# Kernel optimization log

Measured on AMD Instinct MI355X. Metric: run time of the kernel, lower is better.

Reference implementation:

```python
import jax, jax.numpy as jnp
import numpy as np

P = 16; N_SIDE = 14; N_PATCH = 196
ENC_DIM = 1024; ENC_DEPTH = 2; ENC_HEADS = 16; ENC_DH = 64
DEC_DIM = 512; DEC_DEPTH = 1; DEC_HEADS = 8; DEC_DH = 64
NUM_MASKED = int(0.75 * N_PATCH)  # 147


def _ln(x, s, b):
    m = jnp.mean(x, axis=-1, keepdims=True)
    v = jnp.var(x, axis=-1, keepdims=True)
    return (x - m) * jax.lax.rsqrt(v + 1e-5) * s + b


def _mha(x, Wqkv, Wo, heads, dh):
    B, N, _ = x.shape
    q, k, v = jnp.split(x @ Wqkv, 3, axis=-1)
    rs = lambda t: t.reshape(B, N, heads, dh).transpose(0, 2, 1, 3)
    q, k, v = rs(q), rs(k), rs(v)
    scores = jnp.einsum('bhqd,bhkd->bhqk', q, k) / jnp.sqrt(jnp.float32(dh))
    att = jax.nn.softmax(scores, axis=-1)
    o = jnp.einsum('bhqk,bhkd->bhqd', att, v).transpose(0, 2, 1, 3).reshape(B, N, heads * dh)
    return o @ Wo


def _transformer(x, params, depth, heads, dh, lnfs, lnfb):
    (ln1s, ln1b, Wqkv, Wo, ln2s, ln2b, W1, b1, W2, b2) = params
    for i in range(depth):
        x = x + _mha(_ln(x, ln1s[i], ln1b[i]), Wqkv[i], Wo[i], heads, dh)
        h = jax.nn.gelu(_ln(x, ln2s[i], ln2b[i]) @ W1[i] + b1[i])
        x = x + h @ W2[i] + b2[i]
    return _ln(x, lnfs, lnfb)


def setup_inputs() -> dict:
    key = jax.random.key(0)
    ks = jax.random.split(key, 24)
    B = 64
    w = lambda k, s: (jax.random.normal(k, s, jnp.float32) * 0.02)
    E, IE = ENC_DIM, ENC_HEADS * ENC_DH
    D, ID = DEC_DIM, DEC_HEADS * DEC_DH
    d = {}
    d['images'] = jax.random.normal(ks[0], (B, 224, 224, 3), jnp.float32)
    d['rand'] = jax.random.uniform(ks[1], (B, N_PATCH), dtype=jnp.float32)
    d['patch_W'] = w(ks[2], (P * P * 3, E)); d['patch_b'] = jnp.zeros((E,), jnp.float32)
    d['pos_emb'] = w(ks[3], (N_PATCH, E))
    d['enc_ln1s'] = jnp.ones((ENC_DEPTH, E), jnp.float32); d['enc_ln1b'] = jnp.zeros((ENC_DEPTH, E), jnp.float32)
    d['enc_Wqkv'] = w(ks[4], (ENC_DEPTH, E, 3 * IE)); d['enc_Wo'] = w(ks[5], (ENC_DEPTH, IE, E))
    d['enc_ln2s'] = jnp.ones((ENC_DEPTH, E), jnp.float32); d['enc_ln2b'] = jnp.zeros((ENC_DEPTH, E), jnp.float32)
    d['enc_W1'] = w(ks[6], (ENC_DEPTH, E, 4 * E)); d['enc_b1'] = jnp.zeros((ENC_DEPTH, 4 * E), jnp.float32)
    d['enc_W2'] = w(ks[7], (ENC_DEPTH, 4 * E, E)); d['enc_b2'] = jnp.zeros((ENC_DEPTH, E), jnp.float32)
    d['enc_lnfs'] = jnp.ones((E,), jnp.float32); d['enc_lnfb'] = jnp.zeros((E,), jnp.float32)
    d['e2d_W'] = w(ks[8], (E, D)); d['e2d_b'] = jnp.zeros((D,), jnp.float32)
    d['mask_token'] = w(ks[9], (D,))
    d['dec_pos'] = w(ks[10], (N_PATCH, D))
    d['dec_ln1s'] = jnp.ones((DEC_DEPTH, D), jnp.float32); d['dec_ln1b'] = jnp.zeros((DEC_DEPTH, D), jnp.float32)
    d['dec_Wqkv'] = w(ks[11], (DEC_DEPTH, D, 3 * ID)); d['dec_Wo'] = w(ks[12], (DEC_DEPTH, ID, D))
    d['dec_ln2s'] = jnp.ones((DEC_DEPTH, D), jnp.float32); d['dec_ln2b'] = jnp.zeros((DEC_DEPTH, D), jnp.float32)
    d['dec_W1'] = w(ks[13], (DEC_DEPTH, D, 4 * D)); d['dec_b1'] = jnp.zeros((DEC_DEPTH, 4 * D), jnp.float32)
    d['dec_W2'] = w(ks[14], (DEC_DEPTH, 4 * D, D)); d['dec_b2'] = jnp.zeros((DEC_DEPTH, D), jnp.float32)
    d['dec_lnfs'] = jnp.ones((D,), jnp.float32); d['dec_lnfb'] = jnp.zeros((D,), jnp.float32)
    d['pix_W'] = w(ks[15], (D, E)); d['pix_b'] = jnp.zeros((E,), jnp.float32)  # pixel_dim == encoder_dim per source
    return d


def reference(images, rand, patch_W, patch_b, pos_emb,
              enc_ln1s, enc_ln1b, enc_Wqkv, enc_Wo, enc_ln2s, enc_ln2b,
              enc_W1, enc_b1, enc_W2, enc_b2, enc_lnfs, enc_lnfb,
              e2d_W, e2d_b, mask_token, dec_pos,
              dec_ln1s, dec_ln1b, dec_Wqkv, dec_Wo, dec_ln2s, dec_ln2b,
              dec_W1, dec_b1, dec_W2, dec_b2, dec_lnfs, dec_lnfb,
              pix_W, pix_b):
    B = images.shape[0]
    # patch embed: [B,224,224,3] -> [B,196,768] -> [B,196,1024]
    x = images.reshape(B, N_SIDE, P, N_SIDE, P, 3).transpose(0, 1, 3, 2, 4, 5).reshape(B, N_PATCH, P * P * 3)
    patches = x @ patch_W + patch_b
    tokens = patches + pos_emb
    # random masking via argsort of uniform noise
    order = jnp.argsort(rand, axis=-1)
    m_idx = order[:, :NUM_MASKED]        # [B,147]
    u_idx = order[:, NUM_MASKED:]        # [B,49]
    unmasked = jnp.take_along_axis(tokens, u_idx[:, :, None], axis=1)
    enc_params = (enc_ln1s, enc_ln1b, enc_Wqkv, enc_Wo, enc_ln2s, enc_ln2b, enc_W1, enc_b1, enc_W2, enc_b2)
    encoded = _transformer(unmasked, enc_params, ENC_DEPTH, ENC_HEADS, ENC_DH, enc_lnfs, enc_lnfb)
    dec_tok = encoded @ e2d_W + e2d_b + dec_pos[u_idx]
    mask_toks = mask_token + dec_pos[m_idx]
    bidx = jnp.arange(B)[:, None]
    all_tok = jnp.zeros((B, N_PATCH, DEC_DIM), dec_tok.dtype)
    all_tok = all_tok.at[bidx, u_idx].set(dec_tok)
    all_tok = all_tok.at[bidx, m_idx].set(mask_toks)
    dec_params = (dec_ln1s, dec_ln1b, dec_Wqkv, dec_Wo, dec_ln2s, dec_ln2b, dec_W1, dec_b1, dec_W2, dec_b2)
    decoded = _transformer(all_tok, dec_params, DEC_DEPTH, DEC_HEADS, DEC_DH, dec_lnfs, dec_lnfb)
    pred = jnp.take_along_axis(decoded, m_idx[:, :, None], axis=1) @ pix_W + pix_b
    target = jnp.take_along_axis(patches, m_idx[:, :, None], axis=1)
    return jnp.mean((pred - target) ** 2)
```

## Files before the change

kernel.cpp:

```cpp
#include <hip/hip_runtime.h>

typedef __attribute__((ext_vector_type(8))) __bf16 bf16x8;
typedef __attribute__((ext_vector_type(4))) float f32x4;

#define OFF_PATCH 0ull
#define OFF_X     25690112ull
#define OFF_LN    51380224ull
#define OFF_QKV   64225280ull
#define OFF_HID   103022592ull
#define OFF_WP    154402816ull
#define OFF_ORD   214695936ull
#define OFF_PART  214746112ull

#define WP_PATCH   0ull
#define WP_ENC_QKV 786432ull
#define WP_ENC_WO  7077888ull
#define WP_ENC_W1  9175040ull
#define WP_ENC_W2  17563648ull
#define WP_E2D     25952256ull
#define WP_DEC_QKV 26476544ull
#define WP_DEC_WO  27262976ull
#define WP_DEC_W1  27525120ull
#define WP_DEC_W2  28573696ull
#define WP_PIX     29622272ull

#define OM_BF16 0
#define OM_F32  1
#define OM_ACC  2
#define OM_GELU 3

__device__ __forceinline__ float b2f(unsigned short u) {
    return __uint_as_float(((unsigned int)u) << 16);
}
__device__ __forceinline__ unsigned short f2b(float f) {
    unsigned int x = __float_as_uint(f);
    x += 0x7fffu + ((x >> 16) & 1u);
    return (unsigned short)(x >> 16);
}
__device__ __forceinline__ float gelu_f(float x) {
    float u2 = 1.5957691216057308f * x * (1.f + 0.044715f * x * x);
    return x / (1.f + __expf(-u2));
}
__device__ __forceinline__ void gload16(const void* g, void* l) {
    __builtin_amdgcn_global_load_lds((const __attribute__((address_space(1))) void*)g,
                                     (__attribute__((address_space(3))) void*)l, 16, 0, 0);
}

__global__ __launch_bounds__(256) void pack_w(const float* __restrict__ in,
                                              unsigned short* __restrict__ out, int K, int N) {
    __shared__ float tile[32][33];
    int kt = blockIdx.y * 32, nt = blockIdx.x * 32;
    int tx = threadIdx.x & 31, ty = threadIdx.x >> 5;
#pragma unroll
    for (int i = 0; i < 32; i += 8) tile[ty + i][tx] = in[(size_t)(kt + ty + i) * N + nt + tx];
    __syncthreads();
#pragma unroll
    for (int i = 0; i < 32; i += 8)
        out[(size_t)(nt + ty + i) * K + kt + tx] = f2b(tile[tx][ty + i]);
}

__global__ __launch_bounds__(256) void patchify_kernel(const float* __restrict__ img,
                                                       unsigned short* __restrict__ Xp) {
    const long long total = 12544ll * 768;
    for (long long e = (long long)blockIdx.x * 256 + threadIdx.x; e < total;
         e += (long long)gridDim.x * 256) {
        int row = (int)(e / 768), k = (int)(e % 768);
        int b = row / 196, pi = row % 196;
        int py = pi / 14, px = pi % 14;
        int r = k / 48, rem = k % 48;
        int c = rem / 3, ch = rem % 3;
        long long src = (((long long)(b * 224 + py * 16 + r)) * 224 + (px * 16 + c)) * 3 + ch;
        Xp[e] = f2b(img[src]);
    }
}

template <int BT, int NW, int OM>
__global__ __launch_bounds__(NW * 64) void gemm2(const unsigned short* __restrict__ A,
                                                 const unsigned short* __restrict__ Bt,
                                                 void* __restrict__ Cv,
                                                 const float* __restrict__ bias,
                                                 int M, int N, int K) {
    constexpr int WN = (BT == 256) ? 4 : 2;
    constexpr int MR = BT / 32;
    __shared__ __align__(16) unsigned short As[2][BT * 64];
    __shared__ __align__(16) unsigned short Bs[2][BT * 64];
    const int tid = threadIdx.x, wave = tid >> 6, lane = tid & 63;
    const int brow = blockIdx.y * BT, bcol = blockIdx.x * BT;
    const int fr = lane & 15, fq = lane >> 4;
    const int wr = (wave / WN) * (MR * 16);
    const int wc = (wave % WN) * 64;
    const int srow = wave * 32 + (lane >> 3);
    const int sca = ((lane & 7) ^ (lane >> 3)) * 8;
    const unsigned short* Ag = A + (size_t)(brow + srow) * K + sca;
    const unsigned short* Bg = Bt + (size_t)(bcol + srow) * K + sca;

    f32x4 acc[MR][4];
#pragma unroll
    for (int m = 0; m < MR; ++m)
#pragma unroll
        for (int n = 0; n < 4; ++n) acc[m][n] = (f32x4){0.f, 0.f, 0.f, 0.f};

    auto stage = [&](int buf, int k0) {
        unsigned short* AsW = &As[buf][(wave * 32) * 64];
        unsigned short* BsW = &Bs[buf][(wave * 32) * 64];
#pragma unroll
        for (int i = 0; i < 4; ++i) {
            gload16(Ag + (size_t)(i * 8) * K + k0, AsW + i * 8 * 64);
            gload16(Bg + (size_t)(i * 8) * K + k0, BsW + i * 8 * 64);
        }
    };
    auto compute = [&](int buf) {
        const char* ab = (const char*)&As[buf][0];
        const char* bb = (const char*)&Bs[buf][0];
        const int sw = (fr & 7) << 4;
#pragma unroll
        for (int kk = 0; kk < 2; ++kk) {
            bf16x8 af[MR], bf[4];
#pragma unroll
            for (int m = 0; m < MR; ++m)
                af[m] = *(const bf16x8*)(ab + (wr + m * 16 + fr) * 128 +
                                         ((kk * 64 + fq * 16) ^ sw));
#pragma unroll
            for (int n = 0; n < 4; ++n)
                bf[n] = *(const bf16x8*)(bb + (wc + n * 16 + fr) * 128 +
                                         ((kk * 64 + fq * 16) ^ sw));
#pragma unroll
            for (int m = 0; m < MR; ++m)
#pragma unroll
                for (int n = 0; n < 4; ++n)
                    acc[m][n] = __builtin_amdgcn_mfma_f32_16x16x32_bf16(af[m], bf[n],
                                                                       acc[m][n], 0, 0, 0);
        }
    };

    const int nt = K >> 6;
    stage(0, 0);
    __syncthreads();
    int cur = 0;
    for (int t = 0; t < nt - 1; ++t) {
        stage(cur ^ 1, (t + 1) << 6);
        compute(cur);
        __syncthreads();
        cur ^= 1;
    }
    compute(cur);

#pragma unroll
    for (int m = 0; m < MR; ++m) {
        int rb = brow + wr + m * 16 + fq * 4;
#pragma unroll
        for (int r = 0; r < 4; ++r) {
            int row = rb + r;
            if (row < M) {
#pragma unroll
                for (int n = 0; n < 4; ++n) {
                    int col = bcol + wc + n * 16 + fr;
                    float v = acc[m][n][r];
                    if (bias) v += bias[col];
                    size_t o = (size_t)row * N + col;
                    if constexpr (OM == OM_BF16) ((unsigned short*)Cv)[o] = f2b(v);
                    else if constexpr (OM == OM_F32) ((float*)Cv)[o] = v;
                    else if constexpr (OM == OM_ACC) ((float*)Cv)[o] += v;
                    else ((unsigned short*)Cv)[o] = f2b(gelu_f(v));
                }
            }
        }
    }
}

template <int N, int H, int NW>
__global__ __launch_bounds__(NW * 64) void attn_mfma(const unsigned short* __restrict__ qkv,
                                                     unsigned short* __restrict__ out) {
    constexpr int Npad = ((N + 31) / 32) * 32;
    constexpr int NT = Npad / 16;
    constexpr int KS = Npad / 32;
    constexpr int PS = Npad + 8;
    constexpr int SQ = 3 * H * 64, SO = H * 64;
    __shared__ __align__(16) unsigned short Kl[Npad * 64];
    __shared__ __align__(16) unsigned short Vt[64 * PS];
    __shared__ __align__(16) unsigned short Pl[NW * 16 * PS];
    const int b = blockIdx.x / H, h = blockIdx.x % H;
    const unsigned short* base = qkv + (size_t)b * N * SQ;
    const int qoff = h * 64, koff = (H + h) * 64, voff = (2 * H + h) * 64;
    const int tid = threadIdx.x, wave = tid >> 6, lane = tid & 63;
    const int fr = lane & 15, fq = lane >> 4;

    for (int idx = tid; idx < Npad * 8; idx += NW * 64) {
        int row = idx >> 3, ch = idx & 7;
        uint4 v = {0u, 0u, 0u, 0u};
        if (row < N) v = *(const uint4*)(base + (size_t)row * SQ + koff + ch * 8);
        *(uint4*)((char*)Kl + row * 128 + ((ch * 16) ^ ((row & 7) << 4))) = v;
    }
    for (int idx = tid; idx < Npad * 32; idx += NW * 64) {
        int key = idx >> 5, d2 = (idx & 31) * 2;
        unsigned int v = 0;
        if (key < N) v = *(const unsigned int*)(base + (size_t)key * SQ + voff + d2);
        Vt[d2 * PS + key] = (unsigned short)(v & 0xffffu);
        Vt[(d2 + 1) * PS + key] = (unsigned short)(v >> 16);
    }
    __syncthreads();

    unsigned short* pw = Pl + wave * 16 * PS;
    for (int qt = wave; qt < NT; qt += NW) {
        const int q0 = qt * 16;
        int qr = q0 + fr;
        if (qr > N - 1) qr = N - 1;
        const unsigned short* qp = base + (size_t)qr * SQ + qoff + fq * 8;
        bf16x8 aq0 = *(const bf16x8*)qp;
        bf16x8 aq1 = *(const bf16x8*)(qp + 32);
        f32x4 sa[NT];
#pragma unroll
        for (int ct = 0; ct < NT; ++ct) sa[ct] = (f32x4){0.f, 0.f, 0.f, 0.f};
#pragma unroll
        for (int ct = 0; ct < NT; ++ct) {
            const char* kb = (const char*)Kl + (ct * 16 + fr) * 128;
            bf16x8 kf0 = *(const bf16x8*)(kb + ((fq * 16) ^ ((fr & 7) << 4)));
            bf16x8 kf1 = *(const bf16x8*)(kb + ((64 + fq * 16) ^ ((fr & 7) << 4)));
            sa[ct] = __builtin_amdgcn_mfma_f32_16x16x32_bf16(aq0, kf0, sa[ct], 0, 0, 0);
            sa[ct] = __builtin_amdgcn_mfma_f32_16x16x32_bf16(aq1, kf1, sa[ct], 0, 0, 0);
        }
        float mrow[4] = {-3e38f, -3e38f, -3e38f, -3e38f};
#pragma unroll
        for (int ct = 0; ct < NT; ++ct) {
            bool ok = (ct * 16 + fr) < N;
#pragma unroll
            for (int r = 0; r < 4; ++r) {
                float s = ok ? sa[ct][r] * 0.125f : -3e38f;
                sa[ct][r] = s;
                mrow[r] = fmaxf(mrow[r], s);
            }
        }
#pragma unroll
        for (int off = 1; off <= 8; off <<= 1)
#pragma unroll
            for (int r = 0; r < 4; ++r) mrow[r] = fmaxf(mrow[r], __shfl_xor(mrow[r], off));
        float ssum[4] = {0.f, 0.f, 0.f, 0.f};
#pragma unroll
        for (int ct = 0; ct < NT; ++ct)
#pragma unroll
            for (int r = 0; r < 4; ++r) {
                float p = __expf(sa[ct][r] - mrow[r]);
                sa[ct][r] = p;
                ssum[r] += p;
            }
#pragma unroll
        for (int off = 1; off <= 8; off <<= 1)
#pragma unroll
            for (int r = 0; r < 4; ++r) ssum[r] += __shfl_xor(ssum[r], off);
#pragma unroll
        for (int ct = 0; ct < NT; ++ct)
#pragma unroll
            for (int r = 0; r < 4; ++r)
                pw[(fq * 4 + r) * PS + ct * 16 + fr] = f2b(sa[ct][r]);
        f32x4 oa[4];
#pragma unroll
        for (int vt = 0; vt < 4; ++vt) oa[vt] = (f32x4){0.f, 0.f, 0.f, 0.f};
#pragma unroll
        for (int ks = 0; ks < KS; ++ks) {
            bf16x8 pa = *(const bf16x8*)(pw + fr * PS + ks * 32 + fq * 8);
#pragma unroll
            for (int vt = 0; vt < 4; ++vt) {
                bf16x8 vf = *(const bf16x8*)(&Vt[(vt * 16 + fr) * PS + ks * 32 + fq * 8]);
                oa[vt] = __builtin_amdgcn_mfma_f32_16x16x32_bf16(pa, vf, oa[vt], 0, 0, 0);
            }
        }
        float inv[4];
#pragma unroll
        for (int r = 0; r < 4; ++r) inv[r] = 1.f / ssum[r];
#pragma unroll
        for (int vt = 0; vt < 4; ++vt)
#pragma unroll
            for (int r = 0; r < 4; ++r) {
                int q = q0 + fq * 4 + r;
                if (q < N)
                    out[((size_t)b * N + q) * SO + h * 64 + vt * 16 + fr] =
                        f2b(oa[vt][r] * inv[r]);
            }
    }
}

__global__ __launch_bounds__(256) void argsort_kernel(const float* __restrict__ rnd,
                                                      int* __restrict__ ord) {
    __shared__ float vals[196];
    int b = blockIdx.x, t = threadIdx.x;
    if (t < 196) vals[t] = rnd[b * 196 + t];
    __syncthreads();
    if (t < 196) {
        float v = vals[t];
        int rank = 0;
        for (int j = 0; j < 196; ++j) {
            float vj = vals[j];
            rank += (vj < v) || (vj == v && j < t);
        }
        ord[b * 196 + rank] = t;
    }
}

__global__ __launch_bounds__(256) void gather_unmasked(const unsigned short* __restrict__ patches,
                                                       const float* __restrict__ pos,
                                                       const int* __restrict__ ord,
                                                       float* __restrict__ xe) {
    int row = blockIdx.x;
    int b = row / 49, i = row % 49;
    int src = ord[b * 196 + 147 + i];
    const unsigned short* pr = patches + ((size_t)(b * 196 + src) << 10);
    const float* pe = pos + ((size_t)src << 10);
    float* o = xe + ((size_t)row << 10);
    int d = threadIdx.x * 4;
    ushort4 pv = *(const ushort4*)(pr + d);
    float4 p4 = *(const float4*)(pe + d);
    float4 r;
    r.x = b2f(pv.x) + p4.x; r.y = b2f(pv.y) + p4.y;
    r.z = b2f(pv.z) + p4.z; r.w = b2f(pv.w) + p4.w;
    *(float4*)(o + d) = r;
}

template <int L>
__global__ __launch_bounds__(256) void ln_kernel(const float* __restrict__ x,
                                                 unsigned short* __restrict__ y,
                                                 const float* __restrict__ sw,
                                                 const float* __restrict__ bw) {
    __shared__ float red[8];
    const int tid = threadIdx.x;
    const float* xr = x + (size_t)blockIdx.x * L;
    float sum = 0.f, sq = 0.f;
    for (int i = tid * 4; i < L; i += 1024) {
        float4 v = *(const float4*)(xr + i);
        sum += v.x + v.y + v.z + v.w;
        sq += v.x * v.x + v.y * v.y + v.z * v.z + v.w * v.w;
    }
    for (int off = 32; off; off >>= 1) {
        sum += __shfl_xor(sum, off);
        sq += __shfl_xor(sq, off);
    }
    int wave = tid >> 6, lane = tid & 63;
    if (lane == 0) { red[wave] = sum; red[4 + wave] = sq; }
    __syncthreads();
    float ts = red[0] + red[1] + red[2] + red[3];
    float tq = red[4] + red[5] + red[6] + red[7];
    float mean = ts / L;
    float inv = rsqrtf(tq / L - mean * mean + 1e-5f);
    unsigned short* yr = y + (size_t)blockIdx.x * L;
    for (int i = tid * 4; i < L; i += 1024) {
        float4 v = *(const float4*)(xr + i);
        float4 s4 = *(const float4*)(sw + i);
        float4 b4 = *(const float4*)(bw + i);
        ushort4 o;
        o.x = f2b((v.x - mean) * inv * s4.x + b4.x);
        o.y = f2b((v.y - mean) * inv * s4.y + b4.y);
        o.z = f2b((v.z - mean) * inv * s4.z + b4.z);
        o.w = f2b((v.w - mean) * inv * s4.w + b4.w);
        *(ushort4*)(yr + i) = o;
    }
}

__global__ __launch_bounds__(256) void scatter_tokens(const float* __restrict__ dec_tok,
                                                      const float* __restrict__ dec_pos,
                                                      const float* __restrict__ mask_tok,
                                                      const int* __restrict__ ord,
                                                      float* __restrict__ all_tok) {
    int e = blockIdx.x;
    int b = e / 196, i = e % 196;
    int idx = ord[e];
    float* o = all_tok + ((size_t)(b * 196 + idx)) * 512;
    const float* dp = dec_pos + (size_t)idx * 512;
    int d = threadIdx.x * 4;
    if (d < 512) {
        float4 dv = *(const float4*)(dp + d);
        float4 sv;
        if (i < 147) sv = *(const float4*)(mask_tok + d);
        else sv = *(const float4*)(dec_tok + ((size_t)(b * 49 + (i - 147))) * 512 + d);
        float4 r = {sv.x + dv.x, sv.y + dv.y, sv.z + dv.z, sv.w + dv.w};
        *(float4*)(o + d) = r;
    }
}

__global__ __launch_bounds__(256) void gather_masked(const unsigned short* __restrict__ x,
                                                     const int* __restrict__ ord,
                                                     unsigned short* __restrict__ gm) {
    int r = blockIdx.x;
    int b = r / 147, j = r % 147;
    int idx = ord[b * 196 + j];
    const unsigned short* src = x + ((size_t)(b * 196 + idx)) * 512;
    unsigned short* o = gm + (size_t)r * 512;
    int d = threadIdx.x * 4;
    if (d < 512) *(ushort4*)(o + d) = *(const ushort4*)(src + d);
}

__global__ __launch_bounds__(256) void loss_partial(const float* __restrict__ pred,
                                                    const unsigned short* __restrict__ patches,
                                                    const int* __restrict__ ord,
                                                    float* __restrict__ part) {
    __shared__ float red[8];
    float local = 0.f;
    const long long total = 9633792ll;
    for (long long e = (long long)blockIdx.x * 256 + threadIdx.x; e < total; e += 4096ll * 256) {
        int r = (int)(e >> 10), d = (int)(e & 1023);
        int b = r / 147, j = r % 147;
        int idx = ord[b * 196 + j];
        float t = b2f(patches[(((size_t)(b * 196 + idx)) << 10) + d]);
        float df = pred[e] - t;
        local += df * df;
    }
    for (int off = 32; off; off >>= 1) local += __shfl_xor(local, off);
    int wave = threadIdx.x >> 6, lane = threadIdx.x & 63;
    if (lane == 0) red[wave] = local;
    __syncthreads();
    if (threadIdx.x == 0) part[blockIdx.x] = red[0] + red[1] + red[2] + red[3];
}

__global__ __launch_bounds__(256) void loss_final(const float* __restrict__ part,
                                                  float* __restrict__ out) {
    __shared__ float red[8];
    float local = 0.f;
    for (int i = threadIdx.x; i < 4096; i += 256) local += part[i];
    for (int off = 32; off; off >>= 1) local += __shfl_xor(local, off);
    int wave = threadIdx.x >> 6, lane = threadIdx.x & 63;
    if (lane == 0) red[wave] = local;
    __syncthreads();
    if (threadIdx.x == 0) out[0] = (red[0] + red[1] + red[2] + red[3]) / 9633792.0f;
}

extern "C" void kernel_launch(void* const* d_in, const int* in_sizes, int n_in, void* d_out,
                              int out_size, void* d_ws, size_t ws_size, hipStream_t stream) {
    const float* images = (const float*)d_in[0];
    const float* rnd = (const float*)d_in[1];
    const float* patch_W = (const float*)d_in[2];
    const float* patch_b = (const float*)d_in[3];
    const float* pos_emb = (const float*)d_in[4];
    const float* enc_ln1s = (const float*)d_in[5];
    const float* enc_ln1b = (const float*)d_in[6];
    const float* enc_Wqkv = (const float*)d_in[7];
    const float* enc_Wo = (const float*)d_in[8];
    const float* enc_ln2s = (const float*)d_in[9];
    const float* enc_ln2b = (const float*)d_in[10];
    const float* enc_W1 = (const float*)d_in[11];
    const float* enc_b1 = (const float*)d_in[12];
    const float* enc_W2 = (const float*)d_in[13];
    const float* enc_b2 = (const float*)d_in[14];
    const float* enc_lnfs = (const float*)d_in[15];
    const float* enc_lnfb = (const float*)d_in[16];
    const float* e2d_W = (const float*)d_in[17];
    const float* e2d_b = (const float*)d_in[18];
    const float* mask_tok = (const float*)d_in[19];
    const float* dec_pos = (const float*)d_in[20];
    const float* dec_ln1s = (const float*)d_in[21];
    const float* dec_ln1b = (const float*)d_in[22];
    const float* dec_Wqkv = (const float*)d_in[23];
    const float* dec_Wo = (const float*)d_in[24];
    const float* dec_ln2s = (const float*)d_in[25];
    const float* dec_ln2b = (const float*)d_in[26];
    const float* dec_W1 = (const float*)d_in[27];
    const float* dec_b1 = (const float*)d_in[28];
    const float* dec_W2 = (const float*)d_in[29];
    const float* dec_b2 = (const float*)d_in[30];
    const float* dec_lnfs = (const float*)d_in[31];
    const float* dec_lnfb = (const float*)d_in[32];
    const float* pix_W = (const float*)d_in[33];
    const float* pix_b = (const float*)d_in[34];

    char* ws = (char*)d_ws;
    unsigned short* patches = (unsigned short*)(ws + OFF_PATCH);
    float* Rx = (float*)(ws + OFF_X);
    unsigned short* Rln = (unsigned short*)(ws + OFF_LN);
    unsigned short* RqkvB = (unsigned short*)(ws + OFF_QKV);
    float* RqkvF = (float*)(ws + OFF_QKV);
    unsigned short* Rhid = (unsigned short*)(ws + OFF_HID);
    unsigned short* wp = (unsigned short*)(ws + OFF_WP);
    int* ord = (int*)(ws + OFF_ORD);
    float* part = (float*)(ws + OFF_PART);
    float* out = (float*)d_out;

    auto PACK = [&](const float* src, size_t wpo, int K, int N) {
        pack_w<<<dim3(N / 32, K / 32), 256, 0, stream>>>(src, wp + wpo, K, N);
    };
    PACK(patch_W, WP_PATCH, 768, 1024);
    for (int l = 0; l < 2; ++l) {
        PACK(enc_Wqkv + (size_t)l * 1024 * 3072, WP_ENC_QKV + (size_t)l * 3145728, 1024, 3072);
        PACK(enc_Wo + (size_t)l * 1024 * 1024, WP_ENC_WO + (size_t)l * 1048576, 1024, 1024);
        PACK(enc_W1 + (size_t)l * 1024 * 4096, WP_ENC_W1 + (size_t)l * 4194304, 1024, 4096);
        PACK(enc_W2 + (size_t)l * 4096 * 1024, WP_ENC_W2 + (size_t)l * 4194304, 4096, 1024);
    }
    PACK(e2d_W, WP_E2D, 1024, 512);
    PACK(dec_Wqkv, WP_DEC_QKV, 512, 1536);
    PACK(dec_Wo, WP_DEC_WO, 512, 512);
    PACK(dec_W1, WP_DEC_W1, 512, 2048);
    PACK(dec_W2, WP_DEC_W2, 2048, 512);
    PACK(pix_W, WP_PIX, 512, 1024);

    auto GEMM = [&](int om, const unsigned short* A, size_t wpo, void* C, const float* bias,
                    int M, int N, int K) {
        const unsigned short* Bt = wp + wpo;
        int b256 = (N / 256) * ((M + 255) / 256);
        if (b256 >= 192) {
            dim3 g(N / 256, (M + 255) / 256);
            if (om == OM_BF16) gemm2<256, 8, OM_BF16><<<g, 512, 0, stream>>>(A, Bt, C, bias, M, N, K);
            else if (om == OM_F32) gemm2<256, 8, OM_F32><<<g, 512, 0, stream>>>(A, Bt, C, bias, M, N, K);
            else if (om == OM_ACC) gemm2<256, 8, OM_ACC><<<g, 512, 0, stream>>>(A, Bt, C, bias, M, N, K);
            else gemm2<256, 8, OM_GELU><<<g, 512, 0, stream>>>(A, Bt, C, bias, M, N, K);
        } else {
            dim3 g(N / 128, (M + 127) / 128);
            if (om == OM_BF16) gemm2<128, 4, OM_BF16><<<g, 256, 0, stream>>>(A, Bt, C, bias, M, N, K);
            else if (om == OM_F32) gemm2<128, 4, OM_F32><<<g, 256, 0, stream>>>(A, Bt, C, bias, M, N, K);
            else if (om == OM_ACC) gemm2<128, 4, OM_ACC><<<g, 256, 0, stream>>>(A, Bt, C, bias, M, N, K);
            else gemm2<128, 4, OM_GELU><<<g, 256, 0, stream>>>(A, Bt, C, bias, M, N, K);
        }
    };

    patchify_kernel<<<4096, 256, 0, stream>>>(images, Rhid);
    GEMM(OM_BF16, Rhid, WP_PATCH, patches, patch_b, 12544, 1024, 768);
    argsort_kernel<<<64, 256, 0, stream>>>(rnd, ord);
    gather_unmasked<<<3136, 256, 0, stream>>>(patches, pos_emb, ord, Rx);

    for (int l = 0; l < 2; ++l) {
        ln_kernel<1024><<<3136, 256, 0, stream>>>(Rx, Rln, enc_ln1s + l * 1024,
                                                  enc_ln1b + l * 1024);
        GEMM(OM_BF16, Rln, WP_ENC_QKV + (size_t)l * 3145728, RqkvB, nullptr, 3136, 3072, 1024);
        attn_mfma<49, 16, 4><<<64 * 16, 256, 0, stream>>>(RqkvB, Rhid);
        GEMM(OM_ACC, Rhid, WP_ENC_WO + (size_t)l * 1048576, Rx, nullptr, 3136, 1024, 1024);
        ln_kernel<1024><<<3136, 256, 0, stream>>>(Rx, Rln, enc_ln2s + l * 1024,
                                                  enc_ln2b + l * 1024);
        GEMM(OM_GELU, Rln, WP_ENC_W1 + (size_t)l * 4194304, Rhid, enc_b1 + l * 4096, 3136,
             4096, 1024);
        GEMM(OM_ACC, Rhid, WP_ENC_W2 + (size_t)l * 4194304, Rx, enc_b2 + l * 1024, 3136, 1024,
             4096);
    }
    ln_kernel<1024><<<3136, 256, 0, stream>>>(Rx, Rln, enc_lnfs, enc_lnfb);

    GEMM(OM_F32, Rln, WP_E2D, RqkvF, e2d_b, 3136, 512, 1024);
    scatter_tokens<<<12544, 256, 0, stream>>>(RqkvF, dec_pos, mask_tok, ord, Rx);

    ln_kernel<512><<<12544, 256, 0, stream>>>(Rx, Rln, dec_ln1s, dec_ln1b);
    GEMM(OM_BF16, Rln, WP_DEC_QKV, RqkvB, nullptr, 12544, 1536, 512);
    attn_mfma<196, 8, 8><<<64 * 8, 512, 0, stream>>>(RqkvB, Rhid);
    GEMM(OM_ACC, Rhid, WP_DEC_WO, Rx, nullptr, 12544, 512, 512);
    ln_kernel<512><<<12544, 256, 0, stream>>>(Rx, Rln, dec_ln2s, dec_ln2b);
    GEMM(OM_GELU, Rln, WP_DEC_W1, Rhid, dec_b1, 12544, 2048, 512);
    GEMM(OM_ACC, Rhid, WP_DEC_W2, Rx, dec_b2, 12544, 512, 2048);
    ln_kernel<512><<<12544, 256, 0, stream>>>(Rx, Rln, dec_lnfs, dec_lnfb);

    gather_masked<<<9408, 256, 0, stream>>>(Rln, ord, Rhid);
    GEMM(OM_F32, Rhid, WP_PIX, RqkvF, pix_b, 9408, 1024, 512);
    loss_partial<<<4096, 256, 0, stream>>>(RqkvF, patches, ord, part);
    loss_final<<<1, 256, 0, stream>>>(part, out);
}
```

Before: 1.052 ms.

## Add split-K with atomic accumulation, XCD-aware block remap, drop 256 tile path

Every GEMM now uses one 128x128 tile kernel, and the larger 256-tile variant is removed. A grid z dimension splits K for the small-N residual projections (encoder Wo and W2, decoder W2), with partial sums added into the fp32 residual through atomicAdd and bias applied only by the first split. Workgroup IDs are remapped so that consecutive tiles land on the same XCD for better L2 locality. The goal is more workgroups, and so better CU occupancy, on GEMMs that previously produced few tiles. The cost is atomic write traffic and a nondeterministic summation order.

```diff
diff --git a/kernel.cpp b/kernel.cpp
--- a/kernel.cpp
+++ b/kernel.cpp
@@ -74,29 +74,31 @@
     }
 }
 
-template <int BT, int NW, int OM>
-__global__ __launch_bounds__(NW * 64) void gemm2(const unsigned short* __restrict__ A,
-                                                 const unsigned short* __restrict__ Bt,
-                                                 void* __restrict__ Cv,
-                                                 const float* __restrict__ bias,
-                                                 int M, int N, int K) {
-    constexpr int WN = (BT == 256) ? 4 : 2;
-    constexpr int MR = BT / 32;
-    __shared__ __align__(16) unsigned short As[2][BT * 64];
-    __shared__ __align__(16) unsigned short Bs[2][BT * 64];
+template <int OM, bool ATOMIC>
+__global__ __launch_bounds__(256) void gemm2(const unsigned short* __restrict__ A,
+                                             const unsigned short* __restrict__ Bt,
+                                             void* __restrict__ Cv,
+                                             const float* __restrict__ bias,
+                                             int M, int N, int K, int Kc) {
+    __shared__ __align__(16) unsigned short As[2][128 * 64];
+    __shared__ __align__(16) unsigned short Bs[2][128 * 64];
     const int tid = threadIdx.x, wave = tid >> 6, lane = tid & 63;
-    const int brow = blockIdx.y * BT, bcol = blockIdx.x * BT;
+    int nwg = gridDim.x * gridDim.y;
+    int orig = blockIdx.y * gridDim.x + blockIdx.x;
+    int q = nwg >> 3, r8 = nwg & 7, xcd = orig & 7, off = orig >> 3;
+    int wg = (xcd < r8 ? xcd * (q + 1) : r8 * (q + 1) + (xcd - r8) * q) + off;
+    const int brow = (wg / gridDim.x) * 128, bcol = (wg % gridDim.x) * 128;
+    const int kBeg = blockIdx.z * Kc;
     const int fr = lane & 15, fq = lane >> 4;
-    const int wr = (wave / WN) * (MR * 16);
-    const int wc = (wave % WN) * 64;
+    const int wr = (wave >> 1) * 64, wc = (wave & 1) * 64;
     const int srow = wave * 32 + (lane >> 3);
     const int sca = ((lane & 7) ^ (lane >> 3)) * 8;
-    const unsigned short* Ag = A + (size_t)(brow + srow) * K + sca;
-    const unsigned short* Bg = Bt + (size_t)(bcol + srow) * K + sca;
-
-    f32x4 acc[MR][4];
-#pragma unroll
-    for (int m = 0; m < MR; ++m)
+    const unsigned short* Ag = A + (size_t)(brow + srow) * K + kBeg + sca;
+    const unsigned short* Bg = Bt + (size_t)(bcol + srow) * K + kBeg + sca;
+
+    f32x4 acc[4][4];
+#pragma unroll
+    for (int m = 0; m < 4; ++m)
 #pragma unroll
         for (int n = 0; n < 4; ++n) acc[m][n] = (f32x4){0.f, 0.f, 0.f, 0.f};
 
@@ -115,9 +117,9 @@
         const int sw = (fr & 7) << 4;
 #pragma unroll
         for (int kk = 0; kk < 2; ++kk) {
-            bf16x8 af[MR], bf[4];
-#pragma unroll
-            for (int m = 0; m < MR; ++m)
+            bf16x8 af[4], bf[4];
+#pragma unroll
+            for (int m = 0; m < 4; ++m)
                 af[m] = *(const bf16x8*)(ab + (wr + m * 16 + fr) * 128 +
                                          ((kk * 64 + fq * 16) ^ sw));
 #pragma unroll
@@ -125,7 +127,7 @@
                 bf[n] = *(const bf16x8*)(bb + (wc + n * 16 + fr) * 128 +
                                          ((kk * 64 + fq * 16) ^ sw));
 #pragma unroll
-            for (int m = 0; m < MR; ++m)
+            for (int m = 0; m < 4; ++m)
 #pragma unroll
                 for (int n = 0; n < 4; ++n)
                     acc[m][n] = __builtin_amdgcn_mfma_f32_16x16x32_bf16(af[m], bf[n],
@@ -133,7 +135,7 @@
         }
     };
 
-    const int nt = K >> 6;
+    const int nt = Kc >> 6;
     stage(0, 0);
     __syncthreads();
     int cur = 0;
@@ -145,8 +147,9 @@
     }
     compute(cur);
 
-#pragma unroll
-    for (int m = 0; m < MR; ++m) {
+    const bool addBias = (bias != nullptr) && (kBeg == 0);
+#pragma unroll
+    for (int m = 0; m < 4; ++m) {
         int rb = brow + wr + m * 16 + fq * 4;
 #pragma unroll
         for (int r = 0; r < 4; ++r) {
@@ -156,9 +159,10 @@
                 for (int n = 0; n < 4; ++n) {
                     int col = bcol + wc + n * 16 + fr;
                     float v = acc[m][n][r];
-                    if (bias) v += bias[col];
+                    if (addBias) v += bias[col];
                     size_t o = (size_t)row * N + col;
-                    if constexpr (OM == OM_BF16) ((unsigned short*)Cv)[o] = f2b(v);
+                    if constexpr (ATOMIC) atomicAdd((float*)Cv + o, v);
+                    else if constexpr (OM == OM_BF16) ((unsigned short*)Cv)[o] = f2b(v);
                     else if constexpr (OM == OM_F32) ((float*)Cv)[o] = v;
                     else if constexpr (OM == OM_ACC) ((float*)Cv)[o] += v;
                     else ((unsigned short*)Cv)[o] = f2b(gelu_f(v));
@@ -489,58 +493,57 @@
     PACK(pix_W, WP_PIX, 512, 1024);
 
     auto GEMM = [&](int om, const unsigned short* A, size_t wpo, void* C, const float* bias,
-                    int M, int N, int K) {
+                    int M, int N, int K, int S) {
         const unsigned short* Bt = wp + wpo;
-        int b256 = (N / 256) * ((M + 255) / 256);
-        if (b256 >= 192) {
-            dim3 g(N / 256, (M + 255) / 256);
-            if (om == OM_BF16) gemm2<256, 8, OM_BF16><<<g, 512, 0, stream>>>(A, Bt, C, bias, M, N, K);
-            else if (om == OM_F32) gemm2<256, 8, OM_F32><<<g, 512, 0, stream>>>(A, Bt, C, bias, M, N, K);
-            else if (om == OM_ACC) gemm2<256, 8, OM_ACC><<<g, 512, 0, stream>>>(A, Bt, C, bias, M, N, K);
-            else gemm2<256, 8, OM_GELU><<<g, 512, 0, stream>>>(A, Bt, C, bias, M, N, K);
+        dim3 g(N / 128, (M + 127) / 128, S);
+        int Kc = K / S;
+        if (S > 1) {
+            gemm2<OM_ACC, true><<<g, 256, 0, stream>>>(A, Bt, C, bias, M, N, K, Kc);
+        } else if (om == OM_BF16) {
+            gemm2<OM_BF16, false><<<g, 256, 0, stream>>>(A, Bt, C, bias, M, N, K, Kc);
+        } else if (om == OM_F32) {
+            gemm2<OM_F32, false><<<g, 256, 0, stream>>>(A, Bt, C, bias, M, N, K, Kc);
+        } else if (om == OM_ACC) {
+            gemm2<OM_ACC, false><<<g, 256, 0, stream>>>(A, Bt, C, bias, M, N, K, Kc);
         } else {
-            dim3 g(N / 128, (M + 127) / 128);
-            if (om == OM_BF16) gemm2<128, 4, OM_BF16><<<g, 256, 0, stream>>>(A, Bt, C, bias, M, N, K);
-            else if (om == OM_F32) gemm2<128, 4, OM_F32><<<g, 256, 0, stream>>>(A, Bt, C, bias, M, N, K);
-            else if (om == OM_ACC) gemm2<128, 4, OM_ACC><<<g, 256, 0, stream>>>(A, Bt, C, bias, M, N, K);
-            else gemm2<128, 4, OM_GELU><<<g, 256, 0, stream>>>(A, Bt, C, bias, M, N, K);
+            gemm2<OM_GELU, false><<<g, 256, 0, stream>>>(A, Bt, C, bias, M, N, K, Kc);
         }
     };
 
     patchify_kernel<<<4096, 256, 0, stream>>>(images, Rhid);
-    GEMM(OM_BF16, Rhid, WP_PATCH, patches, patch_b, 12544, 1024, 768);
+    GEMM(OM_BF16, Rhid, WP_PATCH, patches, patch_b, 12544, 1024, 768, 1);
     argsort_kernel<<<64, 256, 0, stream>>>(rnd, ord);
     gather_unmasked<<<3136, 256, 0, stream>>>(patches, pos_emb, ord, Rx);
 
     for (int l = 0; l < 2; ++l) {
         ln_kernel<1024><<<3136, 256, 0, stream>>>(Rx, Rln, enc_ln1s + l * 1024,
                                                   enc_ln1b + l * 1024);
-        GEMM(OM_BF16, Rln, WP_ENC_QKV + (size_t)l * 3145728, RqkvB, nullptr, 3136, 3072, 1024);
+        GEMM(OM_BF16, Rln, WP_ENC_QKV + (size_t)l * 3145728, RqkvB, nullptr, 3136, 3072, 1024, 1);
         attn_mfma<49, 16, 4><<<64 * 16, 256, 0, stream>>>(RqkvB, Rhid);
-        GEMM(OM_ACC, Rhid, WP_ENC_WO + (size_t)l * 1048576, Rx, nullptr, 3136, 1024, 1024);
+        GEMM(OM_ACC, Rhid, WP_ENC_WO + (size_t)l * 1048576, Rx, nullptr, 3136, 1024, 1024, 2);
         ln_kernel<1024><<<3136, 256, 0, stream>>>(Rx, Rln, enc_ln2s + l * 1024,
                                                   enc_ln2b + l * 1024);
         GEMM(OM_GELU, Rln, WP_ENC_W1 + (size_t)l * 4194304, Rhid, enc_b1 + l * 4096, 3136,
-             4096, 1024);
+             4096, 1024, 1);
         GEMM(OM_ACC, Rhid, WP_ENC_W2 + (size_t)l * 4194304, Rx, enc_b2 + l * 1024, 3136, 1024,
-             4096);
+             4096, 4);
     }
     ln_kernel<1024><<<3136, 256, 0, stream>>>(Rx, Rln, enc_lnfs, enc_lnfb);
 
-    GEMM(OM_F32, Rln, WP_E2D, RqkvF, e2d_b, 3136, 512, 1024);
+    GEMM(OM_F32, Rln, WP_E2D, RqkvF, e2d_b, 3136, 512, 1024, 1);
     scatter_tokens<<<12544, 256, 0, stream>>>(RqkvF, dec_pos, mask_tok, ord, Rx);
 
     ln_kernel<512><<<12544, 256, 0, stream>>>(Rx, Rln, dec_ln1s, dec_ln1b);
-    GEMM(OM_BF16, Rln, WP_DEC_QKV, RqkvB, nullptr, 12544, 1536, 512);
+    GEMM(OM_BF16, Rln, WP_DEC_QKV, RqkvB, nullptr, 12544, 1536, 512, 1);
     attn_mfma<196, 8, 8><<<64 * 8, 512, 0, stream>>>(RqkvB, Rhid);
-    GEMM(OM_ACC, Rhid, WP_DEC_WO, Rx, nullptr, 12544, 512, 512);
+    GEMM(OM_ACC, Rhid, WP_DEC_WO, Rx, nullptr, 12544, 512, 512, 1);
     ln_kernel<512><<<12544, 256, 0, stream>>>(Rx, Rln, dec_ln2s, dec_ln2b);
-    GEMM(OM_GELU, Rln, WP_DEC_W1, Rhid, dec_b1, 12544, 2048, 512);
-    GEMM(OM_ACC, Rhid, WP_DEC_W2, Rx, dec_b2, 12544, 512, 2048);
+    GEMM(OM_GELU, Rln, WP_DEC_W1, Rhid, dec_b1, 12544, 2048, 512, 1);
+    GEMM(OM_ACC, Rhid, WP_DEC_W2, Rx, dec_b2, 12544, 512, 2048, 2);
     ln_kernel<512><<<12544, 256, 0, stream>>>(Rx, Rln, dec_lnfs, dec_lnfb);
 
     gather_masked<<<9408, 256, 0, stream>>>(Rln, ord, Rhid);
-    GEMM(OM_F32, Rhid, WP_PIX, RqkvF, pix_b, 9408, 1024, 512);
+    GEMM(OM_F32, Rhid, WP_PIX, RqkvF, pix_b, 9408, 1024, 512, 1);
     loss_partial<<<4096, 256, 0, stream>>>(RqkvF, patches, ord, part);
     loss_final<<<1, 256, 0, stream>>>(part, out);
 }
```

Result: faster. 988.6 us (-6.0%).
